# Optimization experiments

Hardware: AMD Instinct MI355X
Metric: run time of the kernel (lower is better)

The kernel has to match this reference:

```python
import jax, jax.numpy as jnp
import numpy as np

B = 65536  # batch of independent scalar inputs
NQ = 6     # qubits -> state shape (B, 2,2,2,2,2,2); qubit 0 = leftmost axis


def _sel(q, bit, controls):
    ix = [slice(None)] * (NQ + 1)
    for cq in controls:
        ix[cq + 1] = 1
    ix[q + 1] = bit
    return tuple(ix)


def _ry(state, q, theta, controls=()):
    """(Controlled-)RY on qubit q. theta: scalar or (B,) array."""
    half = jnp.asarray(theta) * 0.5
    c, s = jnp.cos(half), jnp.sin(half)
    i0, i1 = _sel(q, 0, controls), _sel(q, 1, controls)
    a0, a1 = state[i0], state[i1]
    if c.ndim:  # batched angle -> broadcast over remaining qubit axes
        bs = (c.shape[0],) + (1,) * (a0.ndim - 1)
        c, s = c.reshape(bs), s.reshape(bs)
    state = state.at[i0].set(c * a0 - s * a1)
    return state.at[i1].set(s * a0 + c * a1)


def _y(state, q, controls=()):
    """(Controlled-)Pauli-Y on qubit q: |0>->i|1>, |1>->-i|0>."""
    i0, i1 = _sel(q, 0, controls), _sel(q, 1, controls)
    a0, a1 = state[i0], state[i1]
    state = state.at[i0].set(-1j * a1)
    return state.at[i1].set(1j * a0)


def _circuit(x, p):
    n = x.shape[0]
    st = jnp.zeros((n,) + (2,) * NQ, jnp.complex64)
    st = st.at[(slice(None),) + (0,) * NQ].set(1.0)
    # -- data encoding block 1 --
    st = _ry(st, 0, x * 3.0); st = _ry(st, 1, x * 9.0); st = _ry(st, 2, x)
    # -- variational layer on qubits 0..2 --
    st = _ry(st, 0, p[0]); st = _ry(st, 1, p[1]); st = _ry(st, 2, p[2])
    # -- controlled rotations onto qubits 3,4,5 --
    st = _ry(st, 3, p[3], (2,)); st = _ry(st, 3, p[4], (1,)); st = _ry(st, 3, p[5], (0,)); st = _ry(st, 3, p[6])
    st = _ry(st, 4, p[7], (2,)); st = _ry(st, 4, p[8], (1,)); st = _ry(st, 4, p[9], (0,)); st = _ry(st, 4, p[10])
    st = _ry(st, 5, p[11], (2,)); st = _ry(st, 5, p[12], (1,)); st = _ry(st, 5, p[13], (0,)); st = _ry(st, 5, p[14])
    st = _ry(st, 3, 0.5); st = _ry(st, 4, 0.5); st = _ry(st, 5, 0.5)
    # -- entangling block among qubits 3,4,5 --
    st = _ry(st, 4, p[15], (3,)); st = _ry(st, 5, p[16], (3,))
    st = _ry(st, 3, p[17], (4,)); st = _ry(st, 5, p[18], (4,))
    st = _ry(st, 3, p[19], (5,)); st = _ry(st, 4, p[20], (5,))
    st = _ry(st, 3, p[21]); st = _ry(st, 4, p[22]); st = _ry(st, 5, p[23])
    # -- triply-controlled Y back onto qubits 0..2 --
    st = _y(st, 0, (3, 4, 5)); st = _y(st, 1, (3, 4, 5)); st = _y(st, 2, (3, 4, 5))
    # -- data encoding block 2 --
    st = _ry(st, 0, x * 7.0); st = _ry(st, 1, x * 17.0); st = _ry(st, 2, x)
    st = _ry(st, 0, p[24]); st = _ry(st, 1, p[25]); st = _ry(st, 2, p[26])
    st = _ry(st, 0, -0.5); st = _ry(st, 1, -0.5); st = _ry(st, 2, -0.5)
    # -- entangling block among qubits 0,1,2 --
    st = _ry(st, 1, p[27], (0,)); st = _ry(st, 2, p[28], (0,))
    st = _ry(st, 0, p[29], (1,)); st = _ry(st, 2, p[30], (1,))
    st = _ry(st, 0, p[31], (2,)); st = _ry(st, 1, p[32], (2,))
    st = _ry(st, 0, p[33]); st = _ry(st, 1, p[34]); st = _ry(st, 2, p[35])
    # marginal probabilities of qubits (0,1,2) being 000 / 111
    p000 = jnp.sum(jnp.abs(st[:, 0, 0, 0]) ** 2, axis=(1, 2, 3))
    p111 = jnp.sum(jnp.abs(st[:, 1, 1, 1]) ** 2, axis=(1, 2, 3))
    return (p111 - p000) * 2.0


def setup_inputs() -> dict:
    key = jax.random.key(0)
    k1, k2 = jax.random.split(key)
    inputs = jax.random.uniform(k1, (B,), dtype=jnp.float32)
    params = jax.random.uniform(k2, (36,), dtype=jnp.float32) * (2.0 * np.pi)
    return {"inputs": inputs, "params": params}


def reference(inputs, params):
    return _circuit(inputs, params)
```

## Files before the change

kernel.cpp:

```cpp
#include <hip/hip_runtime.h>


template <int TB, int CM>
__device__ __forceinline__ void ry_g(float* st, float c, float s) {
#pragma unroll
    for (int i = 0; i < 64; ++i) {
        if (i & TB) continue;
        if ((i & CM) != CM) continue;
        float a0 = st[i];
        float a1 = st[i + TB];
        st[i]      = fmaf(c, a0, -s * a1);
        st[i + TB] = fmaf(s, a0,  c * a1);
    }
}

__global__ __launch_bounds__(256) void pnn_kernel(const float* __restrict__ x,
                                                  const float* __restrict__ p,
                                                  float* __restrict__ out,
                                                  int n) {
    int b = blockIdx.x * blockDim.x + threadIdx.x;
    if (b >= n) return;
    float xv = x[b];

    float st[64];
#pragma unroll
    for (int i = 0; i < 64; ++i) st[i] = 0.0f;
    st[0] = 1.0f;

    float c, s;
    auto cs = [&](float th) { __sincosf(th * 0.5f, &s, &c); };

    cs(xv * 3.0f); ry_g<32, 0>(st, c, s);
    cs(xv * 9.0f); ry_g<16, 0>(st, c, s);
    cs(xv);        ry_g<8, 0>(st, c, s);
    cs(p[0]); ry_g<32, 0>(st, c, s);
    cs(p[1]); ry_g<16, 0>(st, c, s);
    cs(p[2]); ry_g<8, 0>(st, c, s);
    cs(p[3]); ry_g<4, 8>(st, c, s);
    cs(p[4]); ry_g<4, 16>(st, c, s);
    cs(p[5]); ry_g<4, 32>(st, c, s);
    cs(p[6]); ry_g<4, 0>(st, c, s);
    cs(p[7]);  ry_g<2, 8>(st, c, s);
    cs(p[8]);  ry_g<2, 16>(st, c, s);
    cs(p[9]);  ry_g<2, 32>(st, c, s);
    cs(p[10]); ry_g<2, 0>(st, c, s);
    cs(p[11]); ry_g<1, 8>(st, c, s);
    cs(p[12]); ry_g<1, 16>(st, c, s);
    cs(p[13]); ry_g<1, 32>(st, c, s);
    cs(p[14]); ry_g<1, 0>(st, c, s);
    cs(0.5f);
    ry_g<4, 0>(st, c, s); ry_g<2, 0>(st, c, s); ry_g<1, 0>(st, c, s);
    cs(p[15]); ry_g<2, 4>(st, c, s);
    cs(p[16]); ry_g<1, 4>(st, c, s);
    cs(p[17]); ry_g<4, 2>(st, c, s);
    cs(p[18]); ry_g<1, 2>(st, c, s);
    cs(p[19]); ry_g<4, 1>(st, c, s);
    cs(p[20]); ry_g<2, 1>(st, c, s);
    cs(p[21]); ry_g<4, 0>(st, c, s);
    cs(p[22]); ry_g<2, 0>(st, c, s);
    cs(p[23]); ry_g<1, 0>(st, c, s);

    {
        float o[8];
#pragma unroll
        for (int j = 0; j < 8; ++j) o[j] = st[8 * j + 7];
        st[8 * 0 + 7] =  o[7];
        st[8 * 1 + 7] = -o[6];
        st[8 * 2 + 7] = -o[5];
        st[8 * 3 + 7] =  o[4];
        st[8 * 4 + 7] = -o[3];
        st[8 * 5 + 7] =  o[2];
        st[8 * 6 + 7] =  o[1];
        st[8 * 7 + 7] = -o[0];
    }

    cs(xv * 7.0f);  ry_g<32, 0>(st, c, s);
    cs(xv * 17.0f); ry_g<16, 0>(st, c, s);
    cs(xv);         ry_g<8, 0>(st, c, s);
    cs(p[24]); ry_g<32, 0>(st, c, s);
    cs(p[25]); ry_g<16, 0>(st, c, s);
    cs(p[26]); ry_g<8, 0>(st, c, s);
    cs(-0.5f);
    ry_g<32, 0>(st, c, s); ry_g<16, 0>(st, c, s); ry_g<8, 0>(st, c, s);
    cs(p[27]); ry_g<16, 32>(st, c, s);
    cs(p[28]); ry_g<8, 32>(st, c, s);
    cs(p[29]); ry_g<32, 16>(st, c, s);
    cs(p[30]); ry_g<8, 16>(st, c, s);
    cs(p[31]); ry_g<32, 8>(st, c, s);
    cs(p[32]); ry_g<16, 8>(st, c, s);
    cs(p[33]); ry_g<32, 0>(st, c, s);
    cs(p[34]); ry_g<16, 0>(st, c, s);
    cs(p[35]); ry_g<8, 0>(st, c, s);

    float p000 = 0.0f, p111 = 0.0f;
#pragma unroll
    for (int i = 0; i < 8; ++i)   p000 = fmaf(st[i], st[i], p000);
#pragma unroll
    for (int i = 56; i < 64; ++i) p111 = fmaf(st[i], st[i], p111);
    out[b] = (p111 - p000) * 2.0f;
}

extern "C" void kernel_launch(void* const* d_in, const int* in_sizes, int n_in,
                              void* d_out, int out_size, void* d_ws, size_t ws_size,
                              hipStream_t stream) {
    const float* x = (const float*)d_in[0];
    const float* p = (const float*)d_in[1];
    float* out = (float*)d_out;
    int n = in_sizes[0];
    int block = 256;
    int grid = (n + block - 1) / block;
    pnn_kernel<<<grid, block, 0, stream>>>(x, p, out, n);
}
```

Baseline: 61.49 us.

## Split each 64-amplitude state across 8 lanes using cross-lane shuffles

Each batch element's 64-float state vector is now spread over 8 threads holding 8 amplitudes each. Gates on qubits 0-2 become xor-shuffles between lanes, and gates on qubits 3-5 stay in registers. Controls on lane bits are applied by selecting c=1, s=0 on inactive lanes. This cuts per-thread register pressure and raises thread-level parallelism, at the cost of 8x the threads, redundant sincos per lane, and shuffle latency.

After: 69.05 us. 12.3% more time.

```diff
diff --git a/kernel.cpp b/kernel.cpp
--- a/kernel.cpp
+++ b/kernel.cpp
@@ -1,103 +1,127 @@
 #include <hip/hip_runtime.h>
 
 
-template <int TB, int CM>
-__device__ __forceinline__ void ry_g(float* st, float c, float s) {
+template <int TB, int CB>
+__device__ __forceinline__ void ry_r(float* st, float c, float s) {
 #pragma unroll
-    for (int i = 0; i < 64; ++i) {
-        if (i & TB) continue;
-        if ((i & CM) != CM) continue;
-        float a0 = st[i];
-        float a1 = st[i + TB];
-        st[i]      = fmaf(c, a0, -s * a1);
-        st[i + TB] = fmaf(s, a0,  c * a1);
+    for (int r = 0; r < 8; ++r) {
+        if (r & TB) continue;
+        if (CB && !(r & CB)) continue;
+        float a0 = st[r], a1 = st[r + TB];
+        st[r]      = fmaf(c, a0, -(s * a1));
+        st[r + TB] = fmaf(s, a0, c * a1);
     }
+}
+
+template <int TB, int LCM>
+__device__ __forceinline__ void gate_r(float* st, int lane, float c, float s) {
+    if (LCM) {
+        bool act = (lane & LCM) == LCM;
+        c = act ? c : 1.0f;
+        s = act ? s : 0.0f;
+    }
+    ry_r<TB, 0>(st, c, s);
+}
+
+template <int XM>
+__device__ __forceinline__ void ry_x(float* st, float c, float ssgn) {
+#pragma unroll
+    for (int r = 0; r < 8; ++r) {
+        float pr = __shfl_xor(st[r], XM);
+        st[r] = fmaf(c, st[r], ssgn * pr);
+    }
+}
+
+template <int XM, int LCM>
+__device__ __forceinline__ void gate_x(float* st, int lane, float c, float s) {
+    float ssgn = (lane & XM) ? s : -s;
+    if (LCM) {
+        bool act = (lane & LCM) == LCM;
+        c = act ? c : 1.0f;
+        ssgn = act ? ssgn : 0.0f;
+    }
+    ry_x<XM>(st, c, ssgn);
 }
 
 __global__ __launch_bounds__(256) void pnn_kernel(const float* __restrict__ x,
                                                   const float* __restrict__ p,
                                                   float* __restrict__ out,
                                                   int n) {
-    int b = blockIdx.x * blockDim.x + threadIdx.x;
-    if (b >= n) return;
-    float xv = x[b];
+    int gtid = blockIdx.x * blockDim.x + threadIdx.x;
+    int e = gtid >> 3;
+    int lane = gtid & 7;
+    if (e >= n) return;
+    float xv = x[e];
 
-    float st[64];
+    float st[8];
 #pragma unroll
-    for (int i = 0; i < 64; ++i) st[i] = 0.0f;
-    st[0] = 1.0f;
+    for (int r = 0; r < 8; ++r) st[r] = 0.0f;
+    if (lane == 0) st[0] = 1.0f;
 
     float c, s;
     auto cs = [&](float th) { __sincosf(th * 0.5f, &s, &c); };
 
-    cs(xv * 3.0f); ry_g<32, 0>(st, c, s);
-    cs(xv * 9.0f); ry_g<16, 0>(st, c, s);
-    cs(xv);        ry_g<8, 0>(st, c, s);
-    cs(p[0]); ry_g<32, 0>(st, c, s);
-    cs(p[1]); ry_g<16, 0>(st, c, s);
-    cs(p[2]); ry_g<8, 0>(st, c, s);
-    cs(p[3]); ry_g<4, 8>(st, c, s);
-    cs(p[4]); ry_g<4, 16>(st, c, s);
-    cs(p[5]); ry_g<4, 32>(st, c, s);
-    cs(p[6]); ry_g<4, 0>(st, c, s);
-    cs(p[7]);  ry_g<2, 8>(st, c, s);
-    cs(p[8]);  ry_g<2, 16>(st, c, s);
-    cs(p[9]);  ry_g<2, 32>(st, c, s);
-    cs(p[10]); ry_g<2, 0>(st, c, s);
-    cs(p[11]); ry_g<1, 8>(st, c, s);
-    cs(p[12]); ry_g<1, 16>(st, c, s);
-    cs(p[13]); ry_g<1, 32>(st, c, s);
-    cs(p[14]); ry_g<1, 0>(st, c, s);
+    cs(xv * 3.0f); gate_x<4, 0>(st, lane, c, s);
+    cs(xv * 9.0f); gate_x<2, 0>(st, lane, c, s);
+    cs(xv);        gate_x<1, 0>(st, lane, c, s);
+    cs(p[0]); gate_x<4, 0>(st, lane, c, s);
+    cs(p[1]); gate_x<2, 0>(st, lane, c, s);
+    cs(p[2]); gate_x<1, 0>(st, lane, c, s);
+    cs(p[3]); gate_r<4, 1>(st, lane, c, s);
+    cs(p[4]); gate_r<4, 2>(st, lane, c, s);
+    cs(p[5]); gate_r<4, 4>(st, lane, c, s);
+    cs(p[6]); gate_r<4, 0>(st, lane, c, s);
+    cs(p[7]);  gate_r<2, 1>(st, lane, c, s);
+    cs(p[8]);  gate_r<2, 2>(st, lane, c, s);
+    cs(p[9]);  gate_r<2, 4>(st, lane, c, s);
+    cs(p[10]); gate_r<2, 0>(st, lane, c, s);
+    cs(p[11]); gate_r<1, 1>(st, lane, c, s);
+    cs(p[12]); gate_r<1, 2>(st, lane, c, s);
+    cs(p[13]); gate_r<1, 4>(st, lane, c, s);
+    cs(p[14]); gate_r<1, 0>(st, lane, c, s);
     cs(0.5f);
-    ry_g<4, 0>(st, c, s); ry_g<2, 0>(st, c, s); ry_g<1, 0>(st, c, s);
-    cs(p[15]); ry_g<2, 4>(st, c, s);
-    cs(p[16]); ry_g<1, 4>(st, c, s);
-    cs(p[17]); ry_g<4, 2>(st, c, s);
-    cs(p[18]); ry_g<1, 2>(st, c, s);
-    cs(p[19]); ry_g<4, 1>(st, c, s);
-    cs(p[20]); ry_g<2, 1>(st, c, s);
-    cs(p[21]); ry_g<4, 0>(st, c, s);
-    cs(p[22]); ry_g<2, 0>(st, c, s);
-    cs(p[23]); ry_g<1, 0>(st, c, s);
+    ry_r<4, 0>(st, c, s); ry_r<2, 0>(st, c, s); ry_r<1, 0>(st, c, s);
+    cs(p[15]); ry_r<2, 4>(st, c, s);
+    cs(p[16]); ry_r<1, 4>(st, c, s);
+    cs(p[17]); ry_r<4, 2>(st, c, s);
+    cs(p[18]); ry_r<1, 2>(st, c, s);
+    cs(p[19]); ry_r<4, 1>(st, c, s);
+    cs(p[20]); ry_r<2, 1>(st, c, s);
+    cs(p[21]); ry_r<4, 0>(st, c, s);
+    cs(p[22]); ry_r<2, 0>(st, c, s);
+    cs(p[23]); ry_r<1, 0>(st, c, s);
 
     {
-        float o[8];
-#pragma unroll
-        for (int j = 0; j < 8; ++j) o[j] = st[8 * j + 7];
-        st[8 * 0 + 7] =  o[7];
-        st[8 * 1 + 7] = -o[6];
-        st[8 * 2 + 7] = -o[5];
-        st[8 * 3 + 7] =  o[4];
-        st[8 * 4 + 7] = -o[3];
-        st[8 * 5 + 7] =  o[2];
-        st[8 * 6 + 7] =  o[1];
-        st[8 * 7 + 7] = -o[0];
+        float ysign = (__popc(lane) & 1) ? -1.0f : 1.0f;
+        float pr = __shfl_xor(st[7], 7);
+        st[7] = ysign * pr;
     }
 
-    cs(xv * 7.0f);  ry_g<32, 0>(st, c, s);
-    cs(xv * 17.0f); ry_g<16, 0>(st, c, s);
-    cs(xv);         ry_g<8, 0>(st, c, s);
-    cs(p[24]); ry_g<32, 0>(st, c, s);
-    cs(p[25]); ry_g<16, 0>(st, c, s);
-    cs(p[26]); ry_g<8, 0>(st, c, s);
+    cs(xv * 7.0f);  gate_x<4, 0>(st, lane, c, s);
+    cs(xv * 17.0f); gate_x<2, 0>(st, lane, c, s);
+    cs(xv);         gate_x<1, 0>(st, lane, c, s);
+    cs(p[24]); gate_x<4, 0>(st, lane, c, s);
+    cs(p[25]); gate_x<2, 0>(st, lane, c, s);
+    cs(p[26]); gate_x<1, 0>(st, lane, c, s);
     cs(-0.5f);
-    ry_g<32, 0>(st, c, s); ry_g<16, 0>(st, c, s); ry_g<8, 0>(st, c, s);
-    cs(p[27]); ry_g<16, 32>(st, c, s);
-    cs(p[28]); ry_g<8, 32>(st, c, s);
-    cs(p[29]); ry_g<32, 16>(st, c, s);
-    cs(p[30]); ry_g<8, 16>(st, c, s);
-    cs(p[31]); ry_g<32, 8>(st, c, s);
-    cs(p[32]); ry_g<16, 8>(st, c, s);
-    cs(p[33]); ry_g<32, 0>(st, c, s);
-    cs(p[34]); ry_g<16, 0>(st, c, s);
-    cs(p[35]); ry_g<8, 0>(st, c, s);
+    gate_x<4, 0>(st, lane, c, s);
+    gate_x<2, 0>(st, lane, c, s);
+    gate_x<1, 0>(st, lane, c, s);
+    cs(p[27]); gate_x<2, 4>(st, lane, c, s);
+    cs(p[28]); gate_x<1, 4>(st, lane, c, s);
+    cs(p[29]); gate_x<4, 2>(st, lane, c, s);
+    cs(p[30]); gate_x<1, 2>(st, lane, c, s);
+    cs(p[31]); gate_x<4, 1>(st, lane, c, s);
+    cs(p[32]); gate_x<2, 1>(st, lane, c, s);
+    cs(p[33]); gate_x<4, 0>(st, lane, c, s);
+    cs(p[34]); gate_x<2, 0>(st, lane, c, s);
+    cs(p[35]); gate_x<1, 0>(st, lane, c, s);
 
-    float p000 = 0.0f, p111 = 0.0f;
+    float psum = 0.0f;
 #pragma unroll
-    for (int i = 0; i < 8; ++i)   p000 = fmaf(st[i], st[i], p000);
-#pragma unroll
-    for (int i = 56; i < 64; ++i) p111 = fmaf(st[i], st[i], p111);
-    out[b] = (p111 - p000) * 2.0f;
+    for (int r = 0; r < 8; ++r) psum = fmaf(st[r], st[r], psum);
+    float other = __shfl_xor(psum, 7);
+    if (lane == 0) out[e] = (other - psum) * 2.0f;
 }
 
 extern "C" void kernel_launch(void* const* d_in, const int* in_sizes, int n_in,
@@ -107,7 +131,8 @@
     const float* p = (const float*)d_in[1];
     float* out = (float*)d_out;
     int n = in_sizes[0];
+    long long threads = (long long)n * 8;
     int block = 256;
-    int grid = (n + block - 1) / block;
+    int grid = (int)((threads + block - 1) / block);
     pnn_kernel<<<grid, block, 0, stream>>>(x, p, out, n);
 }
```
